# Kernel optimization log

Measured on AMD Instinct MI355X. Metric: run time of the kernel, lower is better.

The kernel has to match this reference:

```python
import jax, jax.numpy as jnp
import numpy as np
from jax import lax

KSIZE = 33          # spatially-varying kernel is 33x33
PAD = 16            # ReplicationPad2d(16)
THRESH = 0.0001     # taps with weight <= 1e-4 are skipped (treated as zero)


def setup_inputs() -> dict:
    key = jax.random.key(0)
    k1, k2 = jax.random.split(key)
    inputImg = jax.random.uniform(k1, (1, 3, 256, 256), dtype=jnp.float32)
    Kernels = jax.random.uniform(k2, (1, KSIZE * KSIZE, 256, 256), dtype=jnp.float32)
    return {"inputImg": inputImg, "Kernels": Kernels}


def reference(inputImg, Kernels):
    B, C, H, W = inputImg.shape
    # Replication (edge) padding by 16 on both spatial dims
    padded = jnp.pad(inputImg, ((0, 0), (0, 0), (PAD, PAD), (PAD, PAD)), mode="edge")
    # Extract all 33x33 patches: [B, C*1089, H, W], channel-major then (fh, fw)
    patches = lax.conv_general_dilated_patches(
        padded, (KSIZE, KSIZE), (1, 1), "VALID",
        dimension_numbers=("NCHW", "OIHW", "NCHW"))
    patches = patches.reshape(B, C, KSIZE * KSIZE, H, W)
    # Threshold: original loop skips taps with kernel weight <= 1e-4
    Keff = jnp.where(Kernels > THRESH, Kernels, jnp.zeros_like(Kernels))  # [B, 1089, H, W]
    # Per-pixel dynamic convolution: sum over the 1089 taps
    out = jnp.einsum("bckhw,bkhw->bchw", patches, Keff)
    return out
```

## Files before the change

kernel.cpp:

```cpp
#include <hip/hip_runtime.h>

#define IMG_H 256
#define IMG_W 256
#define IMG_C 3
#define KS 33
#define PAD 16
#define THRESH 1e-4f
#define FH_PER 3

__global__ __launch_bounds__(256, 4)
void reblur_kernel(const float* __restrict__ img,
                   const float* __restrict__ ker,
                   float* __restrict__ out)
{
    const int x = threadIdx.x;
    const int y = blockIdx.x;
    const int chunk = blockIdx.y;
    const int fh0 = chunk * FH_PER;

    const int pix = y * IMG_W + x;
    const int plane = IMG_H * IMG_W;

    const float* kp = ker + (size_t)(fh0 * KS) * plane + pix;

    float a0 = 0.f, a1 = 0.f, a2 = 0.f;
    const int xm = x - PAD;

    #pragma unroll
    for (int dfh = 0; dfh < FH_PER; ++dfh) {
        int yy = y + (fh0 + dfh) - PAD;
        yy = yy < 0 ? 0 : (yy > IMG_H - 1 ? IMG_H - 1 : yy);
        const float* __restrict__ r0 = img + yy * IMG_W;
        const float* __restrict__ r1 = r0 + plane;
        const float* __restrict__ r2 = r1 + plane;
        #pragma unroll
        for (int fw = 0; fw < KS; ++fw) {
            float w = *kp;
            kp += plane;
            int xx = xm + fw;
            xx = xx < 0 ? 0 : (xx > IMG_W - 1 ? IMG_W - 1 : xx);
            float we = (w > THRESH) ? w : 0.f;
            a0 = fmaf(we, r0[xx], a0);
            a1 = fmaf(we, r1[xx], a1);
            a2 = fmaf(we, r2[xx], a2);
        }
    }

    atomicAdd(out + pix,             a0);
    atomicAdd(out + plane + pix,     a1);
    atomicAdd(out + 2 * plane + pix, a2);
}

extern "C" void kernel_launch(void* const* d_in, const int* in_sizes, int n_in,
                              void* d_out, int out_size, void* d_ws, size_t ws_size,
                              hipStream_t stream) {
    const float* img = (const float*)d_in[0];
    const float* ker = (const float*)d_in[1];
    float* out = (float*)d_out;

    hipMemsetAsync(out, 0, (size_t)out_size * sizeof(float), stream);

    dim3 grid(IMG_H, (KS + FH_PER - 1) / FH_PER);
    reblur_kernel<<<grid, IMG_W, 0, stream>>>(img, ker, out);
}
```

Before: 380.8 us.

## Vectorize kernel-weight loads, stage padded image rows in LDS, compute four pixels per thread

Each block now covers four output rows, and each thread computes four adjacent pixels. Kernel weights are read as float4, and replication-padded image rows are staged once into shared memory, with a sliding register window supplying the taps. This is meant to cut global load instruction count and the repeated clamped image gathers. In exchange it uses more registers and adds an LDS fill plus a barrier per block.

```diff
diff --git a/kernel.cpp b/kernel.cpp
--- a/kernel.cpp
+++ b/kernel.cpp
@@ -7,48 +7,118 @@
 #define PAD 16
 #define THRESH 1e-4f
 #define FH_PER 3
+#define ROWS_PER_BLK 4
+#define PADW (IMG_W + 2 * PAD)
+#define NROWS (IMG_C * (ROWS_PER_BLK + FH_PER - 1))
 
 __global__ __launch_bounds__(256, 4)
 void reblur_kernel(const float* __restrict__ img,
                    const float* __restrict__ ker,
                    float* __restrict__ out)
 {
-    const int x = threadIdx.x;
-    const int y = blockIdx.x;
-    const int chunk = blockIdx.y;
-    const int fh0 = chunk * FH_PER;
+    __shared__ float lds[NROWS * PADW];
 
-    const int pix = y * IMG_W + x;
+    const int tid = threadIdx.x;
+    const int y0 = blockIdx.x * ROWS_PER_BLK;
+    const int fh0 = blockIdx.y * FH_PER;
     const int plane = IMG_H * IMG_W;
 
-    const float* kp = ker + (size_t)(fh0 * KS) * plane + pix;
+    const int ybase = y0 + fh0 - PAD;
+    #pragma unroll
+    for (int ch = 0; ch < IMG_C; ++ch) {
+        #pragma unroll
+        for (int rw = 0; rw < ROWS_PER_BLK + FH_PER - 1; ++rw) {
+            int yy = ybase + rw;
+            yy = yy < 0 ? 0 : (yy > IMG_H - 1 ? IMG_H - 1 : yy);
+            const float* __restrict__ src = img + ch * plane + yy * IMG_W;
+            float* dst = lds + (ch * (ROWS_PER_BLK + FH_PER - 1) + rw) * PADW;
+            for (int p = tid; p < PADW; p += 256) {
+                int sc = p - PAD;
+                sc = sc < 0 ? 0 : (sc > IMG_W - 1 ? IMG_W - 1 : sc);
+                dst[p] = src[sc];
+            }
+        }
+    }
+    __syncthreads();
 
-    float a0 = 0.f, a1 = 0.f, a2 = 0.f;
-    const int xm = x - PAD;
+    const int r = tid >> 6;
+    const int l = tid & 63;
+    const int x4 = l << 2;
+    const int y = y0 + r;
+
+    const float4* __restrict__ ker4 = (const float4*)ker;
+    const size_t kbase = (size_t)(fh0 * KS) * (plane / 4) + (size_t)y * (IMG_W / 4) + l;
+
+    float acc[IMG_C][4];
+    #pragma unroll
+    for (int c = 0; c < IMG_C; ++c)
+        #pragma unroll
+        for (int p = 0; p < 4; ++p) acc[c][p] = 0.f;
 
     #pragma unroll
     for (int dfh = 0; dfh < FH_PER; ++dfh) {
-        int yy = y + (fh0 + dfh) - PAD;
-        yy = yy < 0 ? 0 : (yy > IMG_H - 1 ? IMG_H - 1 : yy);
-        const float* __restrict__ r0 = img + yy * IMG_W;
-        const float* __restrict__ r1 = r0 + plane;
-        const float* __restrict__ r2 = r1 + plane;
+        float win[IMG_C][8];
+        int woff[IMG_C];
         #pragma unroll
-        for (int fw = 0; fw < KS; ++fw) {
-            float w = *kp;
-            kp += plane;
-            int xx = xm + fw;
-            xx = xx < 0 ? 0 : (xx > IMG_W - 1 ? IMG_W - 1 : xx);
-            float we = (w > THRESH) ? w : 0.f;
-            a0 = fmaf(we, r0[xx], a0);
-            a1 = fmaf(we, r1[xx], a1);
-            a2 = fmaf(we, r2[xx], a2);
+        for (int c = 0; c < IMG_C; ++c) {
+            woff[c] = (c * (ROWS_PER_BLK + FH_PER - 1) + r + dfh) * PADW + x4;
+            float4 t0 = *(const float4*)&lds[woff[c]];
+            win[c][0] = t0.x; win[c][1] = t0.y; win[c][2] = t0.z; win[c][3] = t0.w;
+        }
+        const size_t kb = kbase + (size_t)(dfh * KS) * (plane / 4);
+
+        #pragma unroll
+        for (int g = 0; g < 8; ++g) {
+            #pragma unroll
+            for (int c = 0; c < IMG_C; ++c) {
+                float4 t1 = *(const float4*)&lds[woff[c] + 4 * (g + 1)];
+                win[c][4] = t1.x; win[c][5] = t1.y; win[c][6] = t1.z; win[c][7] = t1.w;
+            }
+            #pragma unroll
+            for (int j = 0; j < 4; ++j) {
+                const int fw = 4 * g + j;
+                float4 kw = ker4[kb + (size_t)fw * (plane / 4)];
+                float w0 = kw.x > THRESH ? kw.x : 0.f;
+                float w1 = kw.y > THRESH ? kw.y : 0.f;
+                float w2 = kw.z > THRESH ? kw.z : 0.f;
+                float w3 = kw.w > THRESH ? kw.w : 0.f;
+                #pragma unroll
+                for (int c = 0; c < IMG_C; ++c) {
+                    acc[c][0] = fmaf(w0, win[c][j + 0], acc[c][0]);
+                    acc[c][1] = fmaf(w1, win[c][j + 1], acc[c][1]);
+                    acc[c][2] = fmaf(w2, win[c][j + 2], acc[c][2]);
+                    acc[c][3] = fmaf(w3, win[c][j + 3], acc[c][3]);
+                }
+            }
+            #pragma unroll
+            for (int c = 0; c < IMG_C; ++c) {
+                win[c][0] = win[c][4]; win[c][1] = win[c][5];
+                win[c][2] = win[c][6]; win[c][3] = win[c][7];
+            }
+        }
+        {
+            float4 kw = ker4[kb + (size_t)32 * (plane / 4)];
+            float w0 = kw.x > THRESH ? kw.x : 0.f;
+            float w1 = kw.y > THRESH ? kw.y : 0.f;
+            float w2 = kw.z > THRESH ? kw.z : 0.f;
+            float w3 = kw.w > THRESH ? kw.w : 0.f;
+            #pragma unroll
+            for (int c = 0; c < IMG_C; ++c) {
+                acc[c][0] = fmaf(w0, win[c][0], acc[c][0]);
+                acc[c][1] = fmaf(w1, win[c][1], acc[c][1]);
+                acc[c][2] = fmaf(w2, win[c][2], acc[c][2]);
+                acc[c][3] = fmaf(w3, win[c][3], acc[c][3]);
+            }
         }
     }
 
-    atomicAdd(out + pix,             a0);
-    atomicAdd(out + plane + pix,     a1);
-    atomicAdd(out + 2 * plane + pix, a2);
+    float* op = out + y * IMG_W + x4;
+    #pragma unroll
+    for (int c = 0; c < IMG_C; ++c) {
+        #pragma unroll
+        for (int p = 0; p < 4; ++p)
+            atomicAdd(op + c * plane + p, acc[c][p]);
+    }
 }
 
 extern "C" void kernel_launch(void* const* d_in, const int* in_sizes, int n_in,
@@ -60,6 +130,6 @@
 
     hipMemsetAsync(out, 0, (size_t)out_size * sizeof(float), stream);
 
-    dim3 grid(IMG_H, (KS + FH_PER - 1) / FH_PER);
-    reblur_kernel<<<grid, IMG_W, 0, stream>>>(img, ker, out);
+    dim3 grid(IMG_H / ROWS_PER_BLK, KS / FH_PER);
+    reblur_kernel<<<grid, 256, 0, stream>>>(img, ker, out);
 }
```

After: 408.5 us. 7.3% more time.

## Stage image rows in LDS, vectorize two pixels per thread, reduce partials

Applied to the files above, without the earlier changes.

Loads the replication-padded image rows for each block into shared memory, then has each thread compute two adjacent pixels with float2 kernel-weight loads and a register sliding window over the image taps. The atomic accumulation and memset are replaced by per-chunk partial sums written to workspace and summed in a second reduction kernel. This aims to cut global gather traffic, clamping arithmetic and atomic contention. In exchange it adds workspace traffic and an extra launch.

```diff
diff --git a/kernel.cpp b/kernel.cpp
--- a/kernel.cpp
+++ b/kernel.cpp
@@ -1,54 +1,131 @@
 #include <hip/hip_runtime.h>
 
+#define IMG_W 256
 #define IMG_H 256
-#define IMG_W 256
-#define IMG_C 3
 #define KS 33
 #define PAD 16
 #define THRESH 1e-4f
 #define FH_PER 3
+#define NCHUNK 11
+#define RPB 2
+#define PADW (IMG_W + 2 * PAD)
+#define WROWS (RPB + FH_PER - 1)
+#define PLANE (IMG_H * IMG_W)
+#define QROW (IMG_W / 2)
 
-__global__ __launch_bounds__(256, 4)
-void reblur_kernel(const float* __restrict__ img,
-                   const float* __restrict__ ker,
-                   float* __restrict__ out)
+__global__ __launch_bounds__(256, 6)
+void reblur_partial(const float* __restrict__ img,
+                    const float* __restrict__ ker,
+                    float* __restrict__ ws)
 {
-    const int x = threadIdx.x;
-    const int y = blockIdx.x;
-    const int chunk = blockIdx.y;
-    const int fh0 = chunk * FH_PER;
+    __shared__ float lds[3 * WROWS * PADW];
 
-    const int pix = y * IMG_W + x;
-    const int plane = IMG_H * IMG_W;
+    const int tid = threadIdx.x;
+    const int y0 = blockIdx.x * RPB;
+    const int fh0 = blockIdx.y * FH_PER;
 
-    const float* kp = ker + (size_t)(fh0 * KS) * plane + pix;
+    const int ybase = y0 + fh0 - PAD;
+    #pragma unroll
+    for (int row = 0; row < 3 * WROWS; ++row) {
+        const int ch = row >> 2;
+        const int rw = row & (WROWS - 1);
+        int yy = ybase + rw;
+        yy = yy < 0 ? 0 : (yy > IMG_H - 1 ? IMG_H - 1 : yy);
+        const float* __restrict__ src = img + ch * PLANE + yy * IMG_W;
+        float* dst = lds + row * PADW;
+        for (int p = tid; p < PADW; p += 256) {
+            int sc = p - PAD;
+            sc = sc < 0 ? 0 : (sc > IMG_W - 1 ? IMG_W - 1 : sc);
+            dst[p] = src[sc];
+        }
+    }
+    __syncthreads();
 
-    float a0 = 0.f, a1 = 0.f, a2 = 0.f;
-    const int xm = x - PAD;
+    const int r = tid >> 7;
+    const int i = tid & 127;
+    const int y = y0 + r;
+    const int x2 = 2 * i;
 
-    #pragma unroll
+    const float2* __restrict__ ker2 = (const float2*)ker;
+    const size_t kbase = (size_t)(fh0 * KS) * (PLANE / 2) + (size_t)y * QROW + i;
+
+    float a0[3] = {0.f, 0.f, 0.f};
+    float a1[3] = {0.f, 0.f, 0.f};
+
+    #pragma unroll 1
     for (int dfh = 0; dfh < FH_PER; ++dfh) {
-        int yy = y + (fh0 + dfh) - PAD;
-        yy = yy < 0 ? 0 : (yy > IMG_H - 1 ? IMG_H - 1 : yy);
-        const float* __restrict__ r0 = img + yy * IMG_W;
-        const float* __restrict__ r1 = r0 + plane;
-        const float* __restrict__ r2 = r1 + plane;
+        const float* __restrict__ b0 = lds + (0 * WROWS + r + dfh) * PADW + x2;
+        const float* __restrict__ b1 = lds + (1 * WROWS + r + dfh) * PADW + x2;
+        const float* __restrict__ b2 = lds + (2 * WROWS + r + dfh) * PADW + x2;
+        const size_t kb = kbase + (size_t)(dfh * KS) * (PLANE / 2);
+
+        float v[3][4];
+        {
+            float2 t;
+            t = *(const float2*)(b0 + 0); v[0][0] = t.x; v[0][1] = t.y;
+            t = *(const float2*)(b0 + 2); v[0][2] = t.x; v[0][3] = t.y;
+            t = *(const float2*)(b1 + 0); v[1][0] = t.x; v[1][1] = t.y;
+            t = *(const float2*)(b1 + 2); v[1][2] = t.x; v[1][3] = t.y;
+            t = *(const float2*)(b2 + 0); v[2][0] = t.x; v[2][1] = t.y;
+            t = *(const float2*)(b2 + 2); v[2][2] = t.x; v[2][3] = t.y;
+        }
+
         #pragma unroll
-        for (int fw = 0; fw < KS; ++fw) {
-            float w = *kp;
-            kp += plane;
-            int xx = xm + fw;
-            xx = xx < 0 ? 0 : (xx > IMG_W - 1 ? IMG_W - 1 : xx);
-            float we = (w > THRESH) ? w : 0.f;
-            a0 = fmaf(we, r0[xx], a0);
-            a1 = fmaf(we, r1[xx], a1);
-            a2 = fmaf(we, r2[xx], a2);
+        for (int g = 0; g < 16; ++g) {
+            float2 kwa = ker2[kb + (size_t)(2 * g)     * (PLANE / 2)];
+            float2 kwb = ker2[kb + (size_t)(2 * g + 1) * (PLANE / 2)];
+            float wa0 = kwa.x > THRESH ? kwa.x : 0.f;
+            float wa1 = kwa.y > THRESH ? kwa.y : 0.f;
+            float wb0 = kwb.x > THRESH ? kwb.x : 0.f;
+            float wb1 = kwb.y > THRESH ? kwb.y : 0.f;
+            #pragma unroll
+            for (int c = 0; c < 3; ++c) {
+                a0[c] = fmaf(wa0, v[c][0], a0[c]);
+                a1[c] = fmaf(wa1, v[c][1], a1[c]);
+                a0[c] = fmaf(wb0, v[c][1], a0[c]);
+                a1[c] = fmaf(wb1, v[c][2], a1[c]);
+            }
+            #pragma unroll
+            for (int c = 0; c < 3; ++c) { v[c][0] = v[c][2]; v[c][1] = v[c][3]; }
+            if (g < 15) {
+                float2 t;
+                t = *(const float2*)(b0 + 2 * g + 4); v[0][2] = t.x; v[0][3] = t.y;
+                t = *(const float2*)(b1 + 2 * g + 4); v[1][2] = t.x; v[1][3] = t.y;
+                t = *(const float2*)(b2 + 2 * g + 4); v[2][2] = t.x; v[2][3] = t.y;
+            }
+        }
+        {
+            float2 kw = ker2[kb + (size_t)32 * (PLANE / 2)];
+            float w0 = kw.x > THRESH ? kw.x : 0.f;
+            float w1 = kw.y > THRESH ? kw.y : 0.f;
+            #pragma unroll
+            for (int c = 0; c < 3; ++c) {
+                a0[c] = fmaf(w0, v[c][0], a0[c]);
+                a1[c] = fmaf(w1, v[c][1], a1[c]);
+            }
         }
     }
 
-    atomicAdd(out + pix,             a0);
-    atomicAdd(out + plane + pix,     a1);
-    atomicAdd(out + 2 * plane + pix, a2);
+    float* wp = ws + (size_t)(blockIdx.y * 3) * PLANE + (size_t)y * IMG_W + x2;
+    #pragma unroll
+    for (int c = 0; c < 3; ++c) {
+        float2 o; o.x = a0[c]; o.y = a1[c];
+        *(float2*)(wp + (size_t)c * PLANE) = o;
+    }
+}
+
+__global__ __launch_bounds__(256)
+void reduce_partials(const float* __restrict__ ws, float* __restrict__ out)
+{
+    const int gid = blockIdx.x * 256 + threadIdx.x;
+    const float4* __restrict__ w4 = (const float4*)ws;
+    float4 s = w4[gid];
+    #pragma unroll
+    for (int c = 1; c < NCHUNK; ++c) {
+        float4 t = w4[(size_t)c * (3 * PLANE / 4) + gid];
+        s.x += t.x; s.y += t.y; s.z += t.z; s.w += t.w;
+    }
+    ((float4*)out)[gid] = s;
 }
 
 extern "C" void kernel_launch(void* const* d_in, const int* in_sizes, int n_in,
@@ -57,9 +134,9 @@
     const float* img = (const float*)d_in[0];
     const float* ker = (const float*)d_in[1];
     float* out = (float*)d_out;
+    float* ws  = (float*)d_ws;
 
-    hipMemsetAsync(out, 0, (size_t)out_size * sizeof(float), stream);
-
-    dim3 grid(IMG_H, (KS + FH_PER - 1) / FH_PER);
-    reblur_kernel<<<grid, IMG_W, 0, stream>>>(img, ker, out);
+    dim3 grid(IMG_H / RPB, NCHUNK);
+    reblur_partial<<<grid, 256, 0, stream>>>(img, ker, ws);
+    reduce_partials<<<3 * PLANE / 4 / 256, 256, 0, stream>>>(ws, out);
 }
```

Result: no change. 387.4 us (+1.7%).
